# Kernel tuning notes

Hardware: AMD Instinct MI355X
Metric: run time of the kernel (lower is better)

## Reference

```python
import jax, jax.numpy as jnp
import numpy as np


def setup_inputs() -> dict:
    key = jax.random.key(0)
    ks = jax.random.split(key, 9)
    B, C, H, W = 16, 512, 64, 64
    C8 = C // 8
    s_in = 1.0 / np.sqrt(C)
    s_out = 1.0 / np.sqrt(C8)
    return {
        "x": jax.random.normal(ks[0], (B, C, H, W), dtype=jnp.float32),
        "Wq": jax.random.normal(ks[1], (C8, C), dtype=jnp.float32) * s_in,
        "bq": jax.random.normal(ks[2], (C8,), dtype=jnp.float32) * s_in,
        "Wk": jax.random.normal(ks[3], (C8, C), dtype=jnp.float32) * s_in,
        "bk": jax.random.normal(ks[4], (C8,), dtype=jnp.float32) * s_in,
        "Wv": jax.random.normal(ks[5], (C8, C), dtype=jnp.float32) * s_in,
        "bv": jax.random.normal(ks[6], (C8,), dtype=jnp.float32) * s_in,
        "Wo": jax.random.normal(ks[7], (C, C8), dtype=jnp.float32) * s_out,
        "bo": jax.random.normal(ks[8], (C,), dtype=jnp.float32) * s_out,
    }


def reference(x, Wq, bq, Wk, bk, Wv, bv, Wo, bo):
    B, C, H, W = x.shape
    N = H * W
    xf = x.reshape(B, C, N)  # 1x1 conv == channel matmul over flattened spatial
    q = jnp.einsum("oc,bcn->bon", Wq, xf) + bq[None, :, None]  # [B, C8, N]
    k = jnp.einsum("oc,bcn->bon", Wk, xf) + bk[None, :, None]
    v = jnp.einsum("oc,bcn->bon", Wv, xf) + bv[None, :, None]
    energy = jnp.einsum("bcn,bdn->bcd", q, k)  # [B, C8, C8] channel attention
    attn = jax.nn.softmax(energy, axis=-1)
    out = jnp.einsum("bcd,bdn->bcn", attn, v)  # [B, C8, N]
    out = jnp.einsum("oc,bcn->bon", Wo, out) + bo[None, :, None]  # [B, C, N]
    return out.reshape(B, C, H, W)
```

## Files before the change

kernel.cpp:

```cpp
#include <hip/hip_runtime.h>
#include <hip/hip_bf16.h>
#include <cstdint>

#define B_SZ 16
#define C_IN 512
#define C8   64
#define NSP  4096
#define QR   192

typedef __attribute__((ext_vector_type(8))) short s8v;
typedef __attribute__((ext_vector_type(4))) float f4v;

__device__ __forceinline__ void split_bf16(float x, unsigned short& h, unsigned short& l) {
    unsigned int u = __float_as_uint(x);
    h = (unsigned short)(u >> 16);
    float r = x - __uint_as_float(u & 0xffff0000u);
    l = (unsigned short)(__float_as_uint(r) >> 16);
}

__device__ __forceinline__ void split8(const float* v, s8v& h, s8v& l) {
#pragma unroll
    for (int j = 0; j < 8; ++j) {
        unsigned short hh, ll;
        split_bf16(v[j], hh, ll);
        h[j] = (short)hh; l[j] = (short)ll;
    }
}

__global__ __launch_bounds__(256) void k_convW(
    const float* __restrict__ Wq, const float* __restrict__ Wk,
    const float* __restrict__ Wv,
    unsigned short* __restrict__ whi, unsigned short* __restrict__ wlo)
{
    const int o = blockIdx.x;
    const float* src = (o < 64)  ? (Wq + (size_t)o * C_IN)
                     : (o < 128) ? (Wk + (size_t)(o - 64) * C_IN)
                                 : (Wv + (size_t)(o - 128) * C_IN);
    for (int c = threadIdx.x; c < C_IN; c += 256) {
        unsigned short h, l;
        split_bf16(src[c], h, l);
        whi[(size_t)o * C_IN + c] = h;
        wlo[(size_t)o * C_IN + c] = l;
    }
}

__global__ __launch_bounds__(512, 4) void k_qkv_mfma(
    const float* __restrict__ x,
    const unsigned short* __restrict__ whi, const unsigned short* __restrict__ wlo,
    const float* __restrict__ bq, const float* __restrict__ bk,
    const float* __restrict__ bv,
    float* __restrict__ qkv)
{
    __shared__ unsigned short as_h[QR * 32], as_l[QR * 32];
    __shared__ unsigned short xs_h[128 * 32], xs_l[128 * 32];

    const int b  = blockIdx.y;
    const int n0 = blockIdx.x * 128;
    const int t  = threadIdx.x;
    const int w  = t >> 6;
    const int l  = t & 63;
    const int wm = w >> 1;
    const int wn = w & 1;
    const int lm = l & 15;
    const int slot = (((l >> 4) ^ (l & 3)) << 3);

    const int nB    = t & 127;
    const int kgB   = t >> 7;
    const int slotB = ((kgB ^ (nB & 3)) << 3);

    f4v acc[3][4];
#pragma unroll
    for (int i = 0; i < 3; ++i)
#pragma unroll
        for (int j = 0; j < 4; ++j) acc[i][j] = (f4v)0.f;

    const float* xcol = x + ((size_t)b * C_IN) * NSP + n0 + nB;
    float xr[8];
    auto loadB = [&](int K0) {
        const float* s_ = xcol + (size_t)(K0 + kgB * 8) * NSP;
#pragma unroll
        for (int j = 0; j < 8; ++j) xr[j] = s_[(size_t)j * NSP];
    };
    loadB(0);

    for (int it = 0; it < 16; ++it) {
        const int k0 = it * 32;
        __syncthreads();
        {
            unsigned short h[8], lo[8];
#pragma unroll
            for (int j = 0; j < 8; ++j) split_bf16(xr[j], h[j], lo[j]);
            s8v hv, lv;
#pragma unroll
            for (int j = 0; j < 8; ++j) { hv[j] = (short)h[j]; lv[j] = (short)lo[j]; }
            *(s8v*)&xs_h[nB * 32 + slotB] = hv;
            *(s8v*)&xs_l[nB * 32 + slotB] = lv;
        }
        for (int c = t; c < 768; c += 512) {
            const int m = c >> 2, kga = c & 3;
            const int dst = m * 32 + ((kga ^ (m & 3)) << 3);
            const size_t srcoff = (size_t)m * C_IN + k0 + kga * 8;
            *(s8v*)&as_h[dst] = *(const s8v*)&whi[srcoff];
            *(s8v*)&as_l[dst] = *(const s8v*)&wlo[srcoff];
        }
        if (it < 15) loadB(k0 + 32);
        __syncthreads();
        s8v ah[3], al[3], bh[4], bl[4];
#pragma unroll
        for (int fm = 0; fm < 3; ++fm) {
            const int m = wm * 48 + fm * 16 + lm;
            ah[fm] = *(const s8v*)&as_h[m * 32 + slot];
            al[fm] = *(const s8v*)&as_l[m * 32 + slot];
        }
#pragma unroll
        for (int fn = 0; fn < 4; ++fn) {
            const int n = wn * 64 + fn * 16 + lm;
            bh[fn] = *(const s8v*)&xs_h[n * 32 + slot];
            bl[fn] = *(const s8v*)&xs_l[n * 32 + slot];
        }
#pragma unroll
        for (int fm = 0; fm < 3; ++fm)
#pragma unroll
            for (int fn = 0; fn < 4; ++fn) {
                acc[fm][fn] = __builtin_amdgcn_mfma_f32_16x16x32_bf16(
                    ah[fm], bh[fn], acc[fm][fn], 0, 0, 0);
                acc[fm][fn] = __builtin_amdgcn_mfma_f32_16x16x32_bf16(
                    ah[fm], bl[fn], acc[fm][fn], 0, 0, 0);
                acc[fm][fn] = __builtin_amdgcn_mfma_f32_16x16x32_bf16(
                    al[fm], bh[fn], acc[fm][fn], 0, 0, 0);
            }
    }

#pragma unroll
    for (int fm = 0; fm < 3; ++fm) {
        const int row0 = wm * 48 + fm * 16;
        const float* barr = (row0 < 64) ? bq : (row0 < 128) ? bk : bv;
        const int rbase = (row0 & 63) + (l >> 4) * 4;
        const int rowg  = row0 + (l >> 4) * 4;
#pragma unroll
        for (int fn = 0; fn < 4; ++fn) {
            const int col = n0 + wn * 64 + fn * 16 + lm;
            float* dst = qkv + ((size_t)b * QR + rowg) * NSP + col;
#pragma unroll
            for (int r = 0; r < 4; ++r)
                dst[(size_t)r * NSP] = acc[fm][fn][r] + barr[rbase + r];
        }
    }
}

__global__ __launch_bounds__(256) void k_energy_mfma(
    const float* __restrict__ qkv, float* __restrict__ part)
{
    const int b = blockIdx.y, s = blockIdx.x;
    const int t = threadIdx.x, w = t >> 6, l = t & 63;
    const int lm = l & 15, lq = l >> 4;
    const float* qb = qkv + (size_t)b * QR * NSP + (size_t)s * 128;
    const float* kb = qb + (size_t)C8 * NSP;

    f4v acc[4];
#pragma unroll
    for (int fd = 0; fd < 4; ++fd) acc[fd] = (f4v)0.f;

#pragma unroll
    for (int ks = 0; ks < 4; ++ks) {
        const float* qrow = qb + (size_t)(w * 16 + lm) * NSP + ks * 32 + lq * 8;
        float qv[8];
        *(float4*)&qv[0] = *(const float4*)qrow;
        *(float4*)&qv[4] = *(const float4*)(qrow + 4);
        s8v qh, ql_;
        split8(qv, qh, ql_);
#pragma unroll
        for (int fd = 0; fd < 4; ++fd) {
            const float* krow = kb + (size_t)(fd * 16 + lm) * NSP + ks * 32 + lq * 8;
            float kv[8];
            *(float4*)&kv[0] = *(const float4*)krow;
            *(float4*)&kv[4] = *(const float4*)(krow + 4);
            s8v kh, kl_;
            split8(kv, kh, kl_);
            acc[fd] = __builtin_amdgcn_mfma_f32_16x16x32_bf16(qh, kh,  acc[fd], 0, 0, 0);
            acc[fd] = __builtin_amdgcn_mfma_f32_16x16x32_bf16(qh, kl_, acc[fd], 0, 0, 0);
            acc[fd] = __builtin_amdgcn_mfma_f32_16x16x32_bf16(ql_, kh, acc[fd], 0, 0, 0);
        }
    }
    float* pb = part + ((size_t)b * 32 + s) * 4096;
#pragma unroll
    for (int fd = 0; fd < 4; ++fd)
#pragma unroll
        for (int r = 0; r < 4; ++r)
            pb[(w * 16 + lq * 4 + r) * 64 + fd * 16 + lm] = acc[fd][r];
}

__global__ __launch_bounds__(256) void k_softmax(
    const float* __restrict__ part, float* __restrict__ attn)
{
    __shared__ float red[4][64];
    const int cRow = blockIdx.x, b = blockIdx.y;
    const int t = threadIdx.x, d = t & 63, sg = t >> 6;
    const float* p = part + (size_t)b * 32 * 4096 + cRow * 64 + d;
    float s = 0.f;
#pragma unroll
    for (int i = 0; i < 8; ++i) s += p[(size_t)(sg * 8 + i) * 4096];
    red[sg][d] = s;
    __syncthreads();
    if (t < 64) {
        float v = red[0][d] + red[1][d] + red[2][d] + red[3][d];
        float m = v;
#pragma unroll
        for (int off = 32; off; off >>= 1) m = fmaxf(m, __shfl_xor(m, off));
        float e = __expf(v - m);
        float sum = e;
#pragma unroll
        for (int off = 32; off; off >>= 1) sum += __shfl_xor(sum, off);
        attn[((size_t)b * 64 + cRow) * 64 + d] = e / sum;
    }
}

__global__ __launch_bounds__(256) void k_woattn(
    const float* __restrict__ Wo, const float* __restrict__ attn,
    float* __restrict__ Mmat)
{
    __shared__ float wosT[64][68];
    __shared__ float as[64][68];
    const int b  = blockIdx.y;
    const int o0 = blockIdx.x * 64;
    const int t  = threadIdx.x;
    const int td = t & 15, to = t >> 4;
#pragma unroll
    for (int i = 0; i < 4; ++i) {
        int idx = t + 256 * i;
        int r = idx >> 4, q4 = idx & 15;
        float4 w = *reinterpret_cast<const float4*>(
            Wo + (size_t)(o0 + r) * 64 + q4 * 4);
        wosT[q4 * 4 + 0][r] = w.x; wosT[q4 * 4 + 1][r] = w.y;
        wosT[q4 * 4 + 2][r] = w.z; wosT[q4 * 4 + 3][r] = w.w;
        float4 a = *reinterpret_cast<const float4*>(
            attn + ((size_t)b * 64 + r) * 64 + q4 * 4);
        *reinterpret_cast<float4*>(&as[r][q4 * 4]) = a;
    }
    __syncthreads();
    float acc[4][4];
#pragma unroll
    for (int i = 0; i < 4; ++i)
#pragma unroll
        for (int j = 0; j < 4; ++j) acc[i][j] = 0.f;
#pragma unroll 8
    for (int kk = 0; kk < 64; ++kk) {
        float4 wv = *reinterpret_cast<const float4*>(&wosT[kk][to * 4]);
        float4 av = *reinterpret_cast<const float4*>(&as[kk][td * 4]);
        const float wr[4] = {wv.x, wv.y, wv.z, wv.w};
        const float ar[4] = {av.x, av.y, av.z, av.w};
#pragma unroll
        for (int i = 0; i < 4; ++i)
#pragma unroll
            for (int j = 0; j < 4; ++j)
                acc[i][j] = fmaf(wr[i], ar[j], acc[i][j]);
    }
#pragma unroll
    for (int i = 0; i < 4; ++i) {
        float4 ov;
        ov.x = acc[i][0]; ov.y = acc[i][1]; ov.z = acc[i][2]; ov.w = acc[i][3];
        *reinterpret_cast<float4*>(
            Mmat + ((size_t)b * 512 + o0 + to * 4 + i) * 64 + td * 4) = ov;
    }
}

__global__ __launch_bounds__(256) void k_out_mfma(
    const float* __restrict__ qkv, const float* __restrict__ Mmat,
    const float* __restrict__ bo, float* __restrict__ out)
{
    __shared__ unsigned short vsT_h[128 * 64];
    __shared__ unsigned short vsT_l[128 * 64];
    const int b  = blockIdx.z;
    const int o0 = blockIdx.y * 64;
    const int n0 = blockIdx.x * 128;
    const int t  = threadIdx.x;
    const int w  = t >> 6, l = t & 63;
    const int lm = l & 15, lq = l >> 4;

    const float* vb = qkv + ((size_t)b * QR + 128) * NSP;

#pragma unroll
    for (int s = 0; s < 2; ++s)
#pragma unroll
        for (int dd = 0; dd < 16; ++dd) {
            const int d = w + 4 * dd;
            const int n = 64 * s + l;
            float xv = vb[(size_t)d * NSP + n0 + n];
            unsigned short h, lo_;
            split_bf16(xv, h, lo_);
            const int addr = n * 64 + ((((d >> 3) ^ (n & 7))) << 3) + (d & 7);
            vsT_h[addr] = h;
            vsT_l[addr] = lo_;
        }

    s8v ah[4][2], al[4][2];
#pragma unroll
    for (int fo = 0; fo < 4; ++fo)
#pragma unroll
        for (int ks = 0; ks < 2; ++ks) {
            const float* mrow = Mmat + ((size_t)b * 512 + o0 + fo * 16 + lm) * 64
                                + ks * 32 + lq * 8;
            float mv[8];
            *(float4*)&mv[0] = *(const float4*)mrow;
            *(float4*)&mv[4] = *(const float4*)(mrow + 4);
            split8(mv, ah[fo][ks], al[fo][ks]);
        }
    __syncthreads();

    f4v acc[4][2];
#pragma unroll
    for (int fo = 0; fo < 4; ++fo)
#pragma unroll
        for (int fn = 0; fn < 2; ++fn) acc[fo][fn] = (f4v)0.f;

    const int nwbase = w * 32;
#pragma unroll
    for (int ks = 0; ks < 2; ++ks) {
        s8v bh[2], bl[2];
#pragma unroll
        for (int fn = 0; fn < 2; ++fn) {
            const int n = nwbase + fn * 16 + lm;
            const int slot = (ks * 4 + lq) ^ (n & 7);
            const int addr = n * 64 + (slot << 3);
            bh[fn] = *(const s8v*)&vsT_h[addr];
            bl[fn] = *(const s8v*)&vsT_l[addr];
        }
#pragma unroll
        for (int fo = 0; fo < 4; ++fo)
#pragma unroll
            for (int fn = 0; fn < 2; ++fn) {
                acc[fo][fn] = __builtin_amdgcn_mfma_f32_16x16x32_bf16(
                    ah[fo][ks], bh[fn], acc[fo][fn], 0, 0, 0);
                acc[fo][fn] = __builtin_amdgcn_mfma_f32_16x16x32_bf16(
                    ah[fo][ks], bl[fn], acc[fo][fn], 0, 0, 0);
                acc[fo][fn] = __builtin_amdgcn_mfma_f32_16x16x32_bf16(
                    al[fo][ks], bh[fn], acc[fo][fn], 0, 0, 0);
            }
    }

#pragma unroll
    for (int fo = 0; fo < 4; ++fo) {
        const int orow0 = o0 + fo * 16 + lq * 4;
#pragma unroll
        for (int fn = 0; fn < 2; ++fn) {
            const int col = n0 + nwbase + fn * 16 + lm;
            float* dst = out + ((size_t)b * 512 + orow0) * NSP + col;
#pragma unroll
            for (int r = 0; r < 4; ++r)
                dst[(size_t)r * NSP] = acc[fo][fn][r] + bo[orow0 + r];
        }
    }
}

extern "C" void kernel_launch(void* const* d_in, const int* in_sizes, int n_in,
                              void* d_out, int out_size, void* d_ws, size_t ws_size,
                              hipStream_t stream)
{
    const float* x  = (const float*)d_in[0];
    const float* Wq = (const float*)d_in[1];
    const float* bq = (const float*)d_in[2];
    const float* Wk = (const float*)d_in[3];
    const float* bk = (const float*)d_in[4];
    const float* Wv = (const float*)d_in[5];
    const float* bv = (const float*)d_in[6];
    const float* Wo = (const float*)d_in[7];
    const float* bo = (const float*)d_in[8];
    float* out = (float*)d_out;

    float* ws   = (float*)d_ws;
    float* qkv  = ws;
    float* part = qkv  + (size_t)B_SZ * QR * NSP;
    float* attn = part + (size_t)B_SZ * 32 * 64 * 64;
    float* Mmat = attn + (size_t)B_SZ * 64 * 64;

    unsigned short* whi = (unsigned short*)part;
    unsigned short* wlo = whi + (size_t)QR * C_IN;

    k_convW      <<<dim3(QR),          256, 0, stream>>>(Wq, Wk, Wv, whi, wlo);
    k_qkv_mfma   <<<dim3(32, B_SZ),    512, 0, stream>>>(x, whi, wlo, bq, bk, bv, qkv);
    k_energy_mfma<<<dim3(32, B_SZ),    256, 0, stream>>>(qkv, part);
    k_softmax    <<<dim3(64, B_SZ),    256, 0, stream>>>(part, attn);
    k_woattn     <<<dim3(8, B_SZ),     256, 0, stream>>>(Wo, attn, Mmat);
    k_out_mfma   <<<dim3(32, 8, B_SZ), 256, 0, stream>>>(qkv, Mmat, bo, out);
}
```

Measured before the change: 308.6 us.

## Fuse energy into QKV kernel, keep only V in global, presplit Mmat

Measured after the change: 293.7 us. 4.8% less time.

```diff
diff --git a/kernel.cpp b/kernel.cpp
--- a/kernel.cpp
+++ b/kernel.cpp
@@ -25,6 +25,10 @@
         split_bf16(v[j], hh, ll);
         h[j] = (short)hh; l[j] = (short)ll;
     }
+}
+
+__device__ __forceinline__ int eqaddr(int row, int n) {
+    return row * 128 + ((((n >> 2) ^ ((row & 7) << 2)) << 2) | (n & 3));
 }
 
 __global__ __launch_bounds__(256) void k_convW(
@@ -44,37 +48,43 @@
     }
 }
 
-__global__ __launch_bounds__(512, 4) void k_qkv_mfma(
+__global__ __launch_bounds__(512, 4) void k_qkv_en(
     const float* __restrict__ x,
     const unsigned short* __restrict__ whi, const unsigned short* __restrict__ wlo,
     const float* __restrict__ bq, const float* __restrict__ bk,
     const float* __restrict__ bv,
-    float* __restrict__ qkv)
-{
-    __shared__ unsigned short as_h[QR * 32], as_l[QR * 32];
-    __shared__ unsigned short xs_h[128 * 32], xs_l[128 * 32];
+    float* __restrict__ v, float* __restrict__ part)
+{
+    __shared__ __align__(16) unsigned char smem[65536];
+    unsigned short* as_h = (unsigned short*)smem;
+    unsigned short* as_l = as_h + QR * 32;
+    unsigned short* xs_h = as_l + QR * 32;
+    unsigned short* xs_l = xs_h + 128 * 32;
+    float* eq = (float*)smem;
 
     const int b  = blockIdx.y;
-    const int n0 = blockIdx.x * 128;
+    const int s  = blockIdx.x;
+    const int n0 = s * 128;
     const int t  = threadIdx.x;
-    const int w  = t >> 6;
-    const int l  = t & 63;
-    const int wm = w >> 1;
-    const int wn = w & 1;
-    const int lm = l & 15;
-    const int slot = (((l >> 4) ^ (l & 3)) << 3);
-
-    const int nB    = t & 127;
-    const int kgB   = t >> 7;
+    const int w  = t >> 6, l = t & 63;
+    const int wm = w >> 1, wn = w & 1;
+    const int lm = l & 15, lq = l >> 4;
+    const int slot = ((lq ^ (l & 3)) << 3);
+
+    const int nB = t & 127, kgB = t >> 7;
     const int slotB = ((kgB ^ (nB & 3)) << 3);
 
+    const int mW = t >> 2, kgW = t & 3;
+    const int dstW0 = mW * 32 + ((kgW ^ (mW & 3)) << 3);
+    const size_t sW0 = (size_t)mW * C_IN + kgW * 8;
+
     f4v acc[3][4];
 #pragma unroll
     for (int i = 0; i < 3; ++i)
 #pragma unroll
         for (int j = 0; j < 4; ++j) acc[i][j] = (f4v)0.f;
 
-    const float* xcol = x + ((size_t)b * C_IN) * NSP + n0 + nB;
+    const float* xcol = x + (size_t)b * C_IN * NSP + n0 + nB;
     float xr[8];
     auto loadB = [&](int K0) {
         const float* s_ = xcol + (size_t)(K0 + kgB * 8) * NSP;
@@ -86,24 +96,31 @@
     for (int it = 0; it < 16; ++it) {
         const int k0 = it * 32;
         __syncthreads();
+        s8v hv, lv;
         {
-            unsigned short h[8], lo[8];
-#pragma unroll
-            for (int j = 0; j < 8; ++j) split_bf16(xr[j], h[j], lo[j]);
-            s8v hv, lv;
-#pragma unroll
-            for (int j = 0; j < 8; ++j) { hv[j] = (short)h[j]; lv[j] = (short)lo[j]; }
-            *(s8v*)&xs_h[nB * 32 + slotB] = hv;
-            *(s8v*)&xs_l[nB * 32 + slotB] = lv;
-        }
-        for (int c = t; c < 768; c += 512) {
-            const int m = c >> 2, kga = c & 3;
-            const int dst = m * 32 + ((kga ^ (m & 3)) << 3);
-            const size_t srcoff = (size_t)m * C_IN + k0 + kga * 8;
-            *(s8v*)&as_h[dst] = *(const s8v*)&whi[srcoff];
-            *(s8v*)&as_l[dst] = *(const s8v*)&wlo[srcoff];
+            unsigned short h, lo_;
+#pragma unroll
+            for (int j = 0; j < 8; ++j) {
+                split_bf16(xr[j], h, lo_);
+                hv[j] = (short)h; lv[j] = (short)lo_;
+            }
         }
         if (it < 15) loadB(k0 + 32);
+        s8v wh0 = *(const s8v*)&whi[sW0 + k0];
+        s8v wl0 = *(const s8v*)&wlo[sW0 + k0];
+        s8v wh1, wl1;
+        if (t < 256) {
+            wh1 = *(const s8v*)&whi[sW0 + 65536 + k0];
+            wl1 = *(const s8v*)&wlo[sW0 + 65536 + k0];
+        }
+        *(s8v*)&xs_h[nB * 32 + slotB] = hv;
+        *(s8v*)&xs_l[nB * 32 + slotB] = lv;
+        *(s8v*)&as_h[dstW0] = wh0;
+        *(s8v*)&as_l[dstW0] = wl0;
+        if (t < 256) {
+            *(s8v*)&as_h[dstW0 + 4096] = wh1;
+            *(s8v*)&as_l[dstW0 + 4096] = wl1;
+        }
         __syncthreads();
         s8v ah[3], al[3], bh[4], bl[4];
 #pragma unroll
@@ -131,63 +148,75 @@
             }
     }
 
+    __syncthreads();
 #pragma unroll
     for (int fm = 0; fm < 3; ++fm) {
-        const int row0 = wm * 48 + fm * 16;
-        const float* barr = (row0 < 64) ? bq : (row0 < 128) ? bk : bv;
-        const int rbase = (row0 & 63) + (l >> 4) * 4;
-        const int rowg  = row0 + (l >> 4) * 4;
-#pragma unroll
-        for (int fn = 0; fn < 4; ++fn) {
-            const int col = n0 + wn * 64 + fn * 16 + lm;
-            float* dst = qkv + ((size_t)b * QR + rowg) * NSP + col;
-#pragma unroll
-            for (int r = 0; r < 4; ++r)
-                dst[(size_t)r * NSP] = acc[fm][fn][r] + barr[rbase + r];
-        }
-    }
-}
-
-__global__ __launch_bounds__(256) void k_energy_mfma(
-    const float* __restrict__ qkv, float* __restrict__ part)
-{
-    const int b = blockIdx.y, s = blockIdx.x;
-    const int t = threadIdx.x, w = t >> 6, l = t & 63;
-    const int lm = l & 15, lq = l >> 4;
-    const float* qb = qkv + (size_t)b * QR * NSP + (size_t)s * 128;
-    const float* kb = qb + (size_t)C8 * NSP;
-
-    f4v acc[4];
-#pragma unroll
-    for (int fd = 0; fd < 4; ++fd) acc[fd] = (f4v)0.f;
-
+        const int row0f = wm * 48 + fm * 16;
+        const int rbase = row0f + lq * 4;
+        if (row0f >= 128) {
+#pragma unroll
+            for (int fn = 0; fn < 4; ++fn) {
+                const int n = wn * 64 + fn * 16 + lm;
+                float* dst = v + ((size_t)b * 64 + (rbase - 128)) * NSP + n0 + n;
+#pragma unroll
+                for (int r = 0; r < 4; ++r)
+                    dst[(size_t)r * NSP] = acc[fm][fn][r] + bv[rbase - 128 + r];
+            }
+        } else {
+            const float* barr = (row0f < 64) ? bq : bk;
+            const int boff = rbase & 63;
+#pragma unroll
+            for (int fn = 0; fn < 4; ++fn) {
+                const int n = wn * 64 + fn * 16 + lm;
+#pragma unroll
+                for (int r = 0; r < 4; ++r)
+                    eq[eqaddr(rbase + r, n)] = acc[fm][fn][r] + barr[boff + r];
+            }
+        }
+    }
+    __syncthreads();
+
+    const int fc = w >> 1, fd0 = (w & 1) * 2;
+    f4v e0 = (f4v)0.f, e1 = (f4v)0.f;
 #pragma unroll
     for (int ks = 0; ks < 4; ++ks) {
-        const float* qrow = qb + (size_t)(w * 16 + lm) * NSP + ks * 32 + lq * 8;
-        float qv[8];
-        *(float4*)&qv[0] = *(const float4*)qrow;
-        *(float4*)&qv[4] = *(const float4*)(qrow + 4);
+        const int nf = ks * 32 + lq * 8;
+        float qa[8];
+        {
+            const int a0 = eqaddr(fc * 16 + lm, nf);
+            *(float4*)&qa[0] = *(const float4*)&eq[a0];
+            *(float4*)&qa[4] = *(const float4*)&eq[a0 + 4];
+        }
         s8v qh, ql_;
-        split8(qv, qh, ql_);
-#pragma unroll
-        for (int fd = 0; fd < 4; ++fd) {
-            const float* krow = kb + (size_t)(fd * 16 + lm) * NSP + ks * 32 + lq * 8;
-            float kv[8];
-            *(float4*)&kv[0] = *(const float4*)krow;
-            *(float4*)&kv[4] = *(const float4*)(krow + 4);
-            s8v kh, kl_;
-            split8(kv, kh, kl_);
-            acc[fd] = __builtin_amdgcn_mfma_f32_16x16x32_bf16(qh, kh,  acc[fd], 0, 0, 0);
-            acc[fd] = __builtin_amdgcn_mfma_f32_16x16x32_bf16(qh, kl_, acc[fd], 0, 0, 0);
-            acc[fd] = __builtin_amdgcn_mfma_f32_16x16x32_bf16(ql_, kh, acc[fd], 0, 0, 0);
-        }
+        split8(qa, qh, ql_);
+        float ka[8];
+        {
+            const int a0 = eqaddr(64 + fd0 * 16 + lm, nf);
+            *(float4*)&ka[0] = *(const float4*)&eq[a0];
+            *(float4*)&ka[4] = *(const float4*)&eq[a0 + 4];
+        }
+        s8v kh, kl_;
+        split8(ka, kh, kl_);
+        e0 = __builtin_amdgcn_mfma_f32_16x16x32_bf16(qh, kh,  e0, 0, 0, 0);
+        e0 = __builtin_amdgcn_mfma_f32_16x16x32_bf16(qh, kl_, e0, 0, 0, 0);
+        e0 = __builtin_amdgcn_mfma_f32_16x16x32_bf16(ql_, kh, e0, 0, 0, 0);
+        {
+            const int a0 = eqaddr(64 + (fd0 + 1) * 16 + lm, nf);
+            *(float4*)&ka[0] = *(const float4*)&eq[a0];
+            *(float4*)&ka[4] = *(const float4*)&eq[a0 + 4];
+        }
+        split8(ka, kh, kl_);
+        e1 = __builtin_amdgcn_mfma_f32_16x16x32_bf16(qh, kh,  e1, 0, 0, 0);
+        e1 = __builtin_amdgcn_mfma_f32_16x16x32_bf16(qh, kl_, e1, 0, 0, 0);
+        e1 = __builtin_amdgcn_mfma_f32_16x16x32_bf16(ql_, kh, e1, 0, 0, 0);
     }
     float* pb = part + ((size_t)b * 32 + s) * 4096;
 #pragma unroll
-    for (int fd = 0; fd < 4; ++fd)
-#pragma unroll
-        for (int r = 0; r < 4; ++r)
-            pb[(w * 16 + lq * 4 + r) * 64 + fd * 16 + lm] = acc[fd][r];
+    for (int r = 0; r < 4; ++r) {
+        const int c = fc * 16 + lq * 4 + r;
+        pb[c * 64 + fd0 * 16 + lm]        = e0[r];
+        pb[c * 64 + (fd0 + 1) * 16 + lm]  = e1[r];
+    }
 }
 
 __global__ __launch_bounds__(256) void k_softmax(
@@ -217,7 +246,7 @@
 
 __global__ __launch_bounds__(256) void k_woattn(
     const float* __restrict__ Wo, const float* __restrict__ attn,
-    float* __restrict__ Mmat)
+    unsigned short* __restrict__ mhi, unsigned short* __restrict__ mlo)
 {
     __shared__ float wosT[64][68];
     __shared__ float as[64][68];
@@ -257,97 +286,90 @@
     }
 #pragma unroll
     for (int i = 0; i < 4; ++i) {
-        float4 ov;
-        ov.x = acc[i][0]; ov.y = acc[i][1]; ov.z = acc[i][2]; ov.w = acc[i][3];
-        *reinterpret_cast<float4*>(
-            Mmat + ((size_t)b * 512 + o0 + to * 4 + i) * 64 + td * 4) = ov;
-    }
-}
-
-__global__ __launch_bounds__(256) void k_out_mfma(
-    const float* __restrict__ qkv, const float* __restrict__ Mmat,
+        unsigned short h[4], lo4[4];
+#pragma unroll
+        for (int j = 0; j < 4; ++j) split_bf16(acc[i][j], h[j], lo4[j]);
+        const size_t base = ((size_t)b * 512 + o0 + to * 4 + i) * 64 + td * 4;
+        uint2 hp, lp;
+        hp.x = (unsigned)h[0]   | ((unsigned)h[1]   << 16);
+        hp.y = (unsigned)h[2]   | ((unsigned)h[3]   << 16);
+        lp.x = (unsigned)lo4[0] | ((unsigned)lo4[1] << 16);
+        lp.y = (unsigned)lo4[2] | ((unsigned)lo4[3] << 16);
+        *reinterpret_cast<uint2*>(&mhi[base]) = hp;
+        *reinterpret_cast<uint2*>(&mlo[base]) = lp;
+    }
+}
+
+__global__ __launch_bounds__(512, 2) void k_out2(
+    const float* __restrict__ v,
+    const unsigned short* __restrict__ mhi, const unsigned short* __restrict__ mlo,
     const float* __restrict__ bo, float* __restrict__ out)
 {
-    __shared__ unsigned short vsT_h[128 * 64];
-    __shared__ unsigned short vsT_l[128 * 64];
-    const int b  = blockIdx.z;
-    const int o0 = blockIdx.y * 64;
-    const int n0 = blockIdx.x * 128;
+    __shared__ unsigned short vsT_h[64 * 64];
+    __shared__ unsigned short vsT_l[64 * 64];
+    const int b  = blockIdx.y;
+    const int n0 = blockIdx.x * 64;
     const int t  = threadIdx.x;
     const int w  = t >> 6, l = t & 63;
     const int lm = l & 15, lq = l >> 4;
 
-    const float* vb = qkv + ((size_t)b * QR + 128) * NSP;
-
-#pragma unroll
-    for (int s = 0; s < 2; ++s)
-#pragma unroll
-        for (int dd = 0; dd < 16; ++dd) {
-            const int d = w + 4 * dd;
-            const int n = 64 * s + l;
-            float xv = vb[(size_t)d * NSP + n0 + n];
-            unsigned short h, lo_;
-            split_bf16(xv, h, lo_);
-            const int addr = n * 64 + ((((d >> 3) ^ (n & 7))) << 3) + (d & 7);
-            vsT_h[addr] = h;
-            vsT_l[addr] = lo_;
-        }
-
-    s8v ah[4][2], al[4][2];
-#pragma unroll
-    for (int fo = 0; fo < 4; ++fo)
-#pragma unroll
-        for (int ks = 0; ks < 2; ++ks) {
-            const float* mrow = Mmat + ((size_t)b * 512 + o0 + fo * 16 + lm) * 64
-                                + ks * 32 + lq * 8;
-            float mv[8];
-            *(float4*)&mv[0] = *(const float4*)mrow;
-            *(float4*)&mv[4] = *(const float4*)(mrow + 4);
-            split8(mv, ah[fo][ks], al[fo][ks]);
-        }
+#pragma unroll
+    for (int i = 0; i < 8; ++i) {
+        const int d = w * 8 + i;
+        const float xv = v[((size_t)b * 64 + d) * NSP + n0 + l];
+        unsigned short h, lo_;
+        split_bf16(xv, h, lo_);
+        const int addr = l * 64 + ((((d >> 3) ^ (l & 7))) << 3) + (d & 7);
+        vsT_h[addr] = h;
+        vsT_l[addr] = lo_;
+    }
     __syncthreads();
 
-    f4v acc[4][2];
-#pragma unroll
-    for (int fo = 0; fo < 4; ++fo)
-#pragma unroll
-        for (int fn = 0; fn < 2; ++fn) acc[fo][fn] = (f4v)0.f;
-
-    const int nwbase = w * 32;
+    f4v acc[4][4];
+#pragma unroll
+    for (int i = 0; i < 4; ++i)
+#pragma unroll
+        for (int j = 0; j < 4; ++j) acc[i][j] = (f4v)0.f;
+
+    const int obase = w * 64;
 #pragma unroll
     for (int ks = 0; ks < 2; ++ks) {
-        s8v bh[2], bl[2];
-#pragma unroll
-        for (int fn = 0; fn < 2; ++fn) {
-            const int n = nwbase + fn * 16 + lm;
-            const int slot = (ks * 4 + lq) ^ (n & 7);
-            const int addr = n * 64 + (slot << 3);
+        s8v bh[4], bl[4];
+#pragma unroll
+        for (int fn = 0; fn < 4; ++fn) {
+            const int n = fn * 16 + lm;
+            const int addr = n * 64 + ((((ks * 4 + lq) ^ (n & 7))) << 3);
             bh[fn] = *(const s8v*)&vsT_h[addr];
             bl[fn] = *(const s8v*)&vsT_l[addr];
         }
 #pragma unroll
-        for (int fo = 0; fo < 4; ++fo)
-#pragma unroll
-            for (int fn = 0; fn < 2; ++fn) {
+        for (int fo = 0; fo < 4; ++fo) {
+            const int o = obase + fo * 16 + lm;
+            const size_t moff = ((size_t)b * 512 + o) * 64 + ks * 32 + lq * 8;
+            s8v ah  = *(const s8v*)&mhi[moff];
+            s8v al_ = *(const s8v*)&mlo[moff];
+#pragma unroll
+            for (int fn = 0; fn < 4; ++fn) {
                 acc[fo][fn] = __builtin_amdgcn_mfma_f32_16x16x32_bf16(
-                    ah[fo][ks], bh[fn], acc[fo][fn], 0, 0, 0);
+                    ah, bh[fn], acc[fo][fn], 0, 0, 0);
                 acc[fo][fn] = __builtin_amdgcn_mfma_f32_16x16x32_bf16(
-                    ah[fo][ks], bl[fn], acc[fo][fn], 0, 0, 0);
+                    ah, bl[fn], acc[fo][fn], 0, 0, 0);
                 acc[fo][fn] = __builtin_amdgcn_mfma_f32_16x16x32_bf16(
-                    al[fo][ks], bh[fn], acc[fo][fn], 0, 0, 0);
+                    al_, bh[fn], acc[fo][fn], 0, 0, 0);
             }
+        }
     }
 
 #pragma unroll
     for (int fo = 0; fo < 4; ++fo) {
-        const int orow0 = o0 + fo * 16 + lq * 4;
-#pragma unroll
-        for (int fn = 0; fn < 2; ++fn) {
-            const int col = n0 + nwbase + fn * 16 + lm;
-            float* dst = out + ((size_t)b * 512 + orow0) * NSP + col;
+        const int orow = obase + fo * 16 + lq * 4;
+#pragma unroll
+        for (int fn = 0; fn < 4; ++fn) {
+            const int nc = n0 + fn * 16 + lm;
+            float* dst = out + ((size_t)b * 512 + orow) * NSP + nc;
 #pragma unroll
             for (int r = 0; r < 4; ++r)
-                dst[(size_t)r * NSP] = acc[fo][fn][r] + bo[orow0 + r];
+                dst[(size_t)r * NSP] = acc[fo][fn][r] + bo[orow + r];
         }
     }
 }
@@ -368,18 +390,17 @@
     float* out = (float*)d_out;
 
     float* ws   = (float*)d_ws;
-    float* qkv  = ws;
-    float* part = qkv  + (size_t)B_SZ * QR * NSP;
+    float* v    = ws;
+    float* part = v    + (size_t)B_SZ * 64 * NSP;
     float* attn = part + (size_t)B_SZ * 32 * 64 * 64;
-    float* Mmat = attn + (size_t)B_SZ * 64 * 64;
-
-    unsigned short* whi = (unsigned short*)part;
+    unsigned short* mhi = (unsigned short*)(attn + (size_t)B_SZ * 64 * 64);
+    unsigned short* mlo = mhi + (size_t)B_SZ * 512 * 64;
+    unsigned short* whi = mlo + (size_t)B_SZ * 512 * 64;
     unsigned short* wlo = whi + (size_t)QR * C_IN;
 
-    k_convW      <<<dim3(QR),          256, 0, stream>>>(Wq, Wk, Wv, whi, wlo);
-    k_qkv_mfma   <<<dim3(32, B_SZ),    512, 0, stream>>>(x, whi, wlo, bq, bk, bv, qkv);
-    k_energy_mfma<<<dim3(32, B_SZ),    256, 0, stream>>>(qkv, part);
-    k_softmax    <<<dim3(64, B_SZ),    256, 0, stream>>>(part, attn);
-    k_woattn     <<<dim3(8, B_SZ),     256, 0, stream>>>(Wo, attn, Mmat);
-    k_out_mfma   <<<dim3(32, 8, B_SZ), 256, 0, stream>>>(qkv, Mmat, bo, out);
-}
+    k_convW  <<<dim3(QR),      256, 0, stream>>>(Wq, Wk, Wv, whi, wlo);
+    k_qkv_en <<<dim3(32, B_SZ), 512, 0, stream>>>(x, whi, wlo, bq, bk, bv, v, part);
+    k_softmax<<<dim3(64, B_SZ), 256, 0, stream>>>(part, attn);
+    k_woattn <<<dim3(8, B_SZ),  256, 0, stream>>>(Wo, attn, mhi, mlo);
+    k_out2   <<<dim3(64, B_SZ), 512, 0, stream>>>(v, mhi, mlo, bo, out);
+}
```
